# Kernel optimization log

Measured on AMD Instinct MI355X. Metric: run time of the kernel, lower is better.

Reference implementation:

```python
import jax, jax.numpy as jnp
import numpy as np

D_MODEL = 1024
N_HEADS = 16
D_K = D_MODEL // N_HEADS
D_FF = 4096
EPS = 1e-5


def setup_inputs() -> dict:
    key = jax.random.key(0)
    ks = jax.random.split(key, 16)
    s = 0.02
    d, f = D_MODEL, D_FF
    return {
        'ebd_x': jax.random.normal(ks[0], (2, 2048, d), jnp.float32),
        'Wq': jax.random.normal(ks[1], (d, d), jnp.float32) * s,
        'bq': jnp.zeros((d,), jnp.float32),
        'Wk': jax.random.normal(ks[2], (d, d), jnp.float32) * s,
        'bk': jnp.zeros((d,), jnp.float32),
        'Wv': jax.random.normal(ks[3], (d, d), jnp.float32) * s,
        'bv': jnp.zeros((d,), jnp.float32),
        'Wo': jax.random.normal(ks[4], (d, d), jnp.float32) * s,
        'bo': jnp.zeros((d,), jnp.float32),
        'W1': jax.random.normal(ks[5], (d, f), jnp.float32) * s,
        'b1': jnp.zeros((f,), jnp.float32),
        'W2': jax.random.normal(ks[6], (f, d), jnp.float32) * s,
        'b2': jnp.zeros((d,), jnp.float32),
        'g1': jnp.ones((d,), jnp.float32),
        'beta1': jnp.zeros((d,), jnp.float32),
        'g2': jnp.ones((d,), jnp.float32),
        'beta2': jnp.zeros((d,), jnp.float32),
    }


def _layernorm(x, g, b):
    mu = jnp.mean(x, axis=-1, keepdims=True)
    var = jnp.mean(jnp.square(x - mu), axis=-1, keepdims=True)
    return (x - mu) * jax.lax.rsqrt(var + EPS) * g + b


def reference(ebd_x, Wq, bq, Wk, bk, Wv, bv, Wo, bo, W1, b1, W2, b2, g1, beta1, g2, beta2):
    b, L, d = ebd_x.shape
    h, dk = N_HEADS, D_K
    # QKV projections, split heads: (b, h, L, dk)
    q = (ebd_x @ Wq + bq).reshape(b, L, h, dk).transpose(0, 2, 1, 3)
    k = (ebd_x @ Wk + bk).reshape(b, L, h, dk).transpose(0, 2, 1, 3)
    v = (ebd_x @ Wv + bv).reshape(b, L, h, dk).transpose(0, 2, 1, 3)
    scores = jnp.einsum('bhLd,bhld->bhLl', q, k) / jnp.sqrt(jnp.float32(dk))
    attn = jax.nn.softmax(scores, axis=-1)
    attn_v = jnp.einsum('bhLl,bhld->bhLd', attn, v)
    # faithful to source: reshape (b,h,L,dk) -> (b,L,d) WITHOUT transposing back
    attn_v = attn_v.reshape(b, L, d)
    attn_v = attn_v @ Wo + bo
    # dropout is identity in eval mode
    x1 = _layernorm(attn_v + ebd_x, g1, beta1)
    ff = jax.nn.gelu(x1 @ W1 + b1, approximate=False) @ W2 + b2
    return _layernorm(ff + x1, g2, beta2)
```

## Files before the change

### kernel.cpp

```cpp
#include <hip/hip_runtime.h>
#include <hip/hip_bf16.h>
#include <math.h>

typedef __bf16 bhalf;
typedef __bf16 bhalf8 __attribute__((ext_vector_type(8)));
typedef float  floatx4 __attribute__((ext_vector_type(4)));
typedef float  floatx8 __attribute__((ext_vector_type(8)));
typedef unsigned short ushort_t;
typedef unsigned short ushort8 __attribute__((ext_vector_type(8)));

#define MFMA16(a, b, c) __builtin_amdgcn_mfma_f32_16x16x32_bf16((a), (b), (c), 0, 0, 0)

__device__ __forceinline__ void gload_lds16(const bhalf* g, bhalf* l)
{
    __builtin_amdgcn_global_load_lds((const __attribute__((address_space(1))) void*)g,
                                     (__attribute__((address_space(3))) void*)l, 16, 0, 0);
}

enum { EPI_PLAIN = 0, EPI_RES = 1, EPI_GELU = 2, EPI_QKV = 3 };

__global__ __launch_bounds__(256) void detect_dtype(const ushort_t* __restrict__ x,
                                                    int* __restrict__ flag)
{
    __shared__ int tot;
    if (threadIdx.x == 0) tot = 0;
    __syncthreads();
    int cnt = 0;
#pragma unroll
    for (int it = 0; it < 8; ++it) {
        const ushort8 u = *(const ushort8*)(x + ((size_t)(it * 256 + threadIdx.x)) * 8);
#pragma unroll
        for (int j = 0; j < 8; j += 2) {
            const int e = (u[j] >> 7) & 0xFF;
            if (e >= 0x90) ++cnt;
        }
    }
    atomicAdd(&tot, cnt);
    __syncthreads();
    if (threadIdx.x == 0) flag[0] = (tot > 64) ? 1 : 0;
}

__global__ __launch_bounds__(256) void norm_x(const void* __restrict__ s,
                                              bhalf* __restrict__ d,
                                              const int* __restrict__ flag)
{
    const int i = (blockIdx.x * 256 + threadIdx.x) * 8;
    if (*flag) {
        const floatx8 v = *(const floatx8*)((const float*)s + i);
        bhalf8 o;
#pragma unroll
        for (int j = 0; j < 8; ++j) o[j] = (bhalf)v[j];
        *(bhalf8*)(d + i) = o;
    } else {
        *(ushort8*)((ushort_t*)d + i) = *(const ushort8*)((const ushort_t*)s + i);
    }
}

struct Cvt { const void* s; bhalf* d; int n; };
struct CvtArr { Cvt t[10]; };

__global__ __launch_bounds__(256) void norm_vec(CvtArr a, const int* __restrict__ flag)
{
    const Cvt c = a.t[blockIdx.y];
    const int i = (blockIdx.x * 256 + threadIdx.x) * 8;
    if (i >= c.n) return;
    if (*flag) {
        const floatx8 v = *(const floatx8*)((const float*)c.s + i);
        bhalf8 o;
#pragma unroll
        for (int j = 0; j < 8; ++j) o[j] = (bhalf)v[j];
        *(bhalf8*)(c.d + i) = o;
    } else {
        *(ushort8*)((ushort_t*)c.d + i) = *(const ushort8*)((const ushort_t*)c.s + i);
    }
}

struct TDesc { const void* src; bhalf* dst; int R, C; };
struct TDescArr { TDesc t[6]; };

__global__ __launch_bounds__(256) void transpose_all(TDescArr a, const int* __restrict__ flag)
{
    __shared__ bhalf sm[32][33];
    const int id = blockIdx.x;
    TDesc d;
    int rem;
    if (id < 4096)      { d = a.t[id >> 10]; rem = id & 1023; }
    else if (id < 8192) { d = a.t[4];        rem = id - 4096; }
    else                { d = a.t[5];        rem = id - 8192; }
    const int txc = d.C >> 5;
    const int bx = (rem % txc) * 32;
    const int by = (rem / txc) * 32;
    const int tx = threadIdx.x & 31;
    const int ty = threadIdx.x >> 5;
    if (*flag) {
        const float* fin = (const float*)d.src;
#pragma unroll
        for (int i = 0; i < 4; ++i)
            sm[ty + i * 8][tx] = (bhalf)fin[(size_t)(by + ty + i * 8) * d.C + bx + tx];
    } else {
        const bhalf* bin = (const bhalf*)d.src;
#pragma unroll
        for (int i = 0; i < 4; ++i)
            sm[ty + i * 8][tx] = bin[(size_t)(by + ty + i * 8) * d.C + bx + tx];
    }
    __syncthreads();
#pragma unroll
    for (int i = 0; i < 4; ++i)
        d.dst[(size_t)(bx + ty + i * 8) * d.R + by + tx] = sm[tx][ty + i * 8];
}

__global__ __launch_bounds__(256) void vt_transpose(const bhalf* __restrict__ Vw,
                                                    bhalf* __restrict__ Vt)
{
    __shared__ bhalf sm[32][33];
    const int bh = blockIdx.z;
    const int b = bh >> 4, h = bh & 15;
    const int tb = blockIdx.y * 32;
    const int db = blockIdx.x * 32;
    const int tx = threadIdx.x & 31;
    const int ty = threadIdx.x >> 5;
#pragma unroll
    for (int i = 0; i < 4; ++i)
        sm[ty + i * 8][tx] = Vw[(size_t)(b * 2048 + tb + ty + i * 8) * 1024 + h * 64 + db + tx];
    __syncthreads();
#pragma unroll
    for (int i = 0; i < 4; ++i)
        Vt[(size_t)(bh * 64 + db + ty + i * 8) * 2048 + tb + tx] = sm[tx][ty + i * 8];
}

template <int EPI, int TN>
__global__ __launch_bounds__(256) void gemm128(
    const bhalf* __restrict__ A, int lda,
    const bhalf* __restrict__ BT, int ldb,
    const bhalf* __restrict__ bias,
    const bhalf* __restrict__ resid,
    bhalf* __restrict__ C, int ldc, int K,
    bhalf* __restrict__ Ck, bhalf* __restrict__ Cv)
{
    __shared__ __align__(16) bhalf As[128 * 64];
    __shared__ __align__(16) bhalf Bs[TN * 64];

    const int tid  = threadIdx.x;
    const int lane = tid & 63;
    const int w    = tid >> 6;
    const int l15  = lane & 15;
    const int q    = lane >> 4;
    constexpr int MT = (TN == 128) ? 4 : 2;
    const int wm   = (TN == 128) ? (w >> 1) * 64 : w * 32;
    const int wn   = (TN == 128) ? (w & 1) * 64 : 0;
    const int n0   = blockIdx.x * TN;
    const int m0   = blockIdx.y * 128;

    const int r8 = lane >> 3;
    const int c8 = lane & 7;
    const int gc = (c8 ^ r8) << 3;

    floatx4 acc[MT][4];
#pragma unroll
    for (int i = 0; i < MT; ++i)
#pragma unroll
        for (int j = 0; j < 4; ++j) acc[i][j] = (floatx4){0.f, 0.f, 0.f, 0.f};

    for (int k0 = 0; k0 < K; k0 += 64) {
        __syncthreads();
#pragma unroll
        for (int i = 0; i < 4; ++i) {
            const int rb = w * 32 + i * 8;
            gload_lds16(A + (size_t)(m0 + rb + r8) * lda + k0 + gc, &As[rb * 64] + lane * 8);
        }
        if constexpr (TN == 128) {
#pragma unroll
            for (int i = 0; i < 4; ++i) {
                const int rb = w * 32 + i * 8;
                gload_lds16(BT + (size_t)(n0 + rb + r8) * ldb + k0 + gc, &Bs[rb * 64] + lane * 8);
            }
        } else {
#pragma unroll
            for (int i = 0; i < 2; ++i) {
                const int rb = w * 16 + i * 8;
                gload_lds16(BT + (size_t)(n0 + rb + r8) * ldb + k0 + gc, &Bs[rb * 64] + lane * 8);
            }
        }
        __syncthreads();
#pragma unroll
        for (int s = 0; s < 2; ++s) {
            const int pc = (((s * 4 + q) ^ (l15 & 7)) << 3);
            bhalf8 af[MT], bf[4];
#pragma unroll
            for (int mt = 0; mt < MT; ++mt)
                af[mt] = *(const bhalf8*)&As[(wm + mt * 16 + l15) * 64 + pc];
#pragma unroll
            for (int nt = 0; nt < 4; ++nt)
                bf[nt] = *(const bhalf8*)&Bs[(wn + nt * 16 + l15) * 64 + pc];
#pragma unroll
            for (int mt = 0; mt < MT; ++mt)
#pragma unroll
                for (int nt = 0; nt < 4; ++nt)
                    acc[mt][nt] = MFMA16(af[mt], bf[nt], acc[mt][nt]);
        }
    }

#pragma unroll
    for (int mt = 0; mt < MT; ++mt)
#pragma unroll
        for (int nt = 0; nt < 4; ++nt) {
            const int col = n0 + wn + nt * 16 + l15;
            const float bv = (float)bias[col];
#pragma unroll
            for (int r = 0; r < 4; ++r) {
                const int row = m0 + wm + mt * 16 + q * 4 + r;
                float v = acc[mt][nt][r] + bv;
                if constexpr (EPI == EPI_PLAIN) {
                    C[(size_t)row * ldc + col] = (bhalf)v;
                } else if constexpr (EPI == EPI_RES) {
                    v += (float)resid[(size_t)row * ldc + col];
                    C[(size_t)row * ldc + col] = (bhalf)v;
                } else if constexpr (EPI == EPI_GELU) {
                    v = 0.5f * v * (1.f + erff(v * 0.70710678118654752f));
                    C[(size_t)row * ldc + col] = (bhalf)v;
                } else {
                    if (col < 1024)       C [(size_t)row * 1024 + col]        = (bhalf)v;
                    else if (col < 2048)  Ck[(size_t)row * 1024 + col - 1024] = (bhalf)v;
                    else                  Cv[(size_t)row * 1024 + col - 2048] = (bhalf)v;
                }
            }
        }
}

template <int EPI>
__global__ __launch_bounds__(512, 2) void gemm256(
    const bhalf* __restrict__ A, int lda,
    const bhalf* __restrict__ BT, int ldb,
    const bhalf* __restrict__ bias,
    bhalf* __restrict__ C, int ldc, int K, int nbx,
    bhalf* __restrict__ Ck, bhalf* __restrict__ Cv)
{
    extern __shared__ __align__(16) bhalf sm[];

    const int tid  = threadIdx.x;
    const int lane = tid & 63;
    const int w    = tid >> 6;
    const int l15  = lane & 15;
    const int q    = lane >> 4;
    const int wm   = (w >> 2) * 128;
    const int wn   = (w & 3) * 64;
    const int w8   = w * 8;

    const int nwg = gridDim.x;
    const int cpx = nwg >> 3;
    const int id  = (blockIdx.x & 7) * cpx + (blockIdx.x >> 3);
    const int bx  = id % nbx;
    const int by  = id / nbx;
    const int n0  = bx * 256;
    const int m0  = by * 256;

    const int r8 = lane >> 3;
    const int c8 = lane & 7;
    const int gc = (c8 ^ r8) << 3;

    floatx4 acc[8][4];
#pragma unroll
    for (int i = 0; i < 8; ++i)
#pragma unroll
        for (int j = 0; j < 4; ++j) acc[i][j] = (floatx4){0.f, 0.f, 0.f, 0.f};

    auto stage = [&](int buf, int k0) {
        bhalf* as = sm + buf * 16384;
        bhalf* bs = sm + 32768 + buf * 16384;
#pragma unroll
        for (int i = 0; i < 4; ++i) {
            const int rb = i * 64 + w8;
            gload_lds16(A  + (size_t)(m0 + rb + r8) * lda + k0 + gc, as + rb * 64 + lane * 8);
            gload_lds16(BT + (size_t)(n0 + rb + r8) * ldb + k0 + gc, bs + rb * 64 + lane * 8);
        }
    };

    stage(0, 0);
    const int NT = K >> 6;
    for (int t = 0; t < NT; ++t) {
        const int cur = t & 1;
        const bhalf* as = sm + cur * 16384;
        const bhalf* bs = sm + 32768 + cur * 16384;
        __syncthreads();
        if (t + 1 < NT) stage(cur ^ 1, (t + 1) << 6);

#pragma unroll
        for (int ks = 0; ks < 2; ++ks) {
            const int pc = ((ks * 4 + q) ^ (l15 & 7)) << 3;
            bhalf8 bf[4];
#pragma unroll
            for (int nt = 0; nt < 4; ++nt)
                bf[nt] = *(const bhalf8*)&bs[(wn + nt * 16 + l15) * 64 + pc];
#pragma unroll
            for (int mh = 0; mh < 2; ++mh) {
                bhalf8 af[4];
#pragma unroll
                for (int mt = 0; mt < 4; ++mt)
                    af[mt] = *(const bhalf8*)&as[(wm + mh * 64 + mt * 16 + l15) * 64 + pc];
#pragma unroll
                for (int mt = 0; mt < 4; ++mt)
#pragma unroll
                    for (int nt = 0; nt < 4; ++nt)
                        acc[mh * 4 + mt][nt] = MFMA16(af[mt], bf[nt], acc[mh * 4 + mt][nt]);
            }
        }
    }

#pragma unroll
    for (int j = 0; j < 8; ++j)
#pragma unroll
        for (int nt = 0; nt < 4; ++nt) {
            const int col = n0 + wn + nt * 16 + l15;
            const float bv = (float)bias[col];
#pragma unroll
            for (int r = 0; r < 4; ++r) {
                const int row = m0 + wm + (j >> 2) * 64 + (j & 3) * 16 + q * 4 + r;
                float v = acc[j][nt][r] + bv;
                if constexpr (EPI == EPI_GELU) {
                    v = 0.5f * v * (1.f + erff(v * 0.70710678118654752f));
                    C[(size_t)row * ldc + col] = (bhalf)v;
                } else if constexpr (EPI == EPI_QKV) {
                    if (col < 1024)       C [(size_t)row * 1024 + col]        = (bhalf)v;
                    else if (col < 2048)  Ck[(size_t)row * 1024 + col - 1024] = (bhalf)v;
                    else                  Cv[(size_t)row * 1024 + col - 2048] = (bhalf)v;
                } else {
                    C[(size_t)row * ldc + col] = (bhalf)v;
                }
            }
        }
}

__global__ __launch_bounds__(256) void flash_attn(
    const bhalf* __restrict__ Q, const bhalf* __restrict__ Km,
    const bhalf* __restrict__ Vt, bhalf* __restrict__ ctx)
{
    __shared__ __align__(16) bhalf Ks[2][64 * 64];
    __shared__ __align__(16) bhalf Vs[2][64 * 64];

    const int tid  = threadIdx.x;
    const int lane = tid & 63;
    const int wq   = tid >> 6;
    const int l15  = lane & 15;
    const int q    = lane >> 4;
    const int bh   = blockIdx.x & 31;
    const int l0   = (blockIdx.x >> 5) * 64;
    const int b    = bh >> 4, h = bh & 15;
    const float SC = 0.125f * 1.44269504f;

    const bhalf* qp = Q + ((size_t)(b * 2048 + l0 + wq * 16 + l15)) * 1024 + h * 64 + q * 8;
    const bhalf8 aQ0 = *(const bhalf8*)qp;
    const bhalf8 aQ1 = *(const bhalf8*)(qp + 32);

    float ps = 0.f;
    floatx4 o[4];
#pragma unroll
    for (int ot = 0; ot < 4; ++ot) o[ot] = (floatx4){0.f, 0.f, 0.f, 0.f};

    const int r8 = lane >> 3;
    const int c8 = lane & 7;
    const bhalf* kbase = Km + ((size_t)(b * 2048)) * 1024 + h * 64;
    const bhalf* vbase = Vt + ((size_t)(bh * 64)) * 2048;

    auto stage = [&](int buf, int kt) {
#pragma unroll
        for (int i = 0; i < 2; ++i) {
            const int rb = wq * 16 + i * 8;
            const int fk = (((rb >> 3) << 1) ^ r8) & 7;
            gload_lds16(kbase + (size_t)(kt + rb + r8) * 1024 + ((c8 ^ fk) << 3),
                        &Ks[buf][rb * 64] + lane * 8);
            gload_lds16(vbase + (size_t)(rb + r8) * 2048 + kt + ((c8 ^ r8) << 3),
                        &Vs[buf][rb * 64] + lane * 8);
        }
    };

    stage(0, 0);
    int cur = 0;
    for (int kt = 0; kt < 2048; kt += 64) {
        __syncthreads();
        if (kt + 64 < 2048) stage(cur ^ 1, kt + 64);

        floatx4 s[4];
#pragma unroll
        for (int nt = 0; nt < 4; ++nt) {
            const int row = (nt >> 1) * 32 + (nt & 1) * 4 + ((l15 >> 2) << 3) + (l15 & 3);
            const int f = (((row >> 3) << 1) ^ row) & 7;
            const bhalf8 k0 = *(const bhalf8*)&Ks[cur][row * 64 + ((q ^ f) << 3)];
            const bhalf8 k1 = *(const bhalf8*)&Ks[cur][row * 64 + (((4 + q) ^ f) << 3)];
            floatx4 z = (floatx4){0.f, 0.f, 0.f, 0.f};
            z = MFMA16(k0, aQ0, z);
            s[nt] = MFMA16(k1, aQ1, z);
        }

        bhalf8 pa[2];
#pragma unroll
        for (int nt = 0; nt < 4; ++nt)
#pragma unroll
            for (int r = 0; r < 4; ++r) {
                const float pv = __builtin_amdgcn_exp2f(fmaf(s[nt][r], SC, -8.f));
                ps += pv;
                pa[nt >> 1][(nt & 1) * 4 + r] = (bhalf)pv;
            }

#pragma unroll
        for (int kc = 0; kc < 2; ++kc)
#pragma unroll
            for (int ot = 0; ot < 4; ++ot) {
                const bhalf8 bV = *(const bhalf8*)&Vs[cur][(ot * 16 + l15) * 64 + (((kc * 4 + q) ^ (l15 & 7)) << 3)];
                o[ot] = MFMA16(pa[kc], bV, o[ot]);
            }
        cur ^= 1;
    }

    ps += __shfl_xor(ps, 16);
    ps += __shfl_xor(ps, 32);
    const float invq = 1.f / ps;
    float inv[4];
#pragma unroll
    for (int r = 0; r < 4; ++r)
        inv[r] = __shfl(invq, (lane & 48) | (q * 4 + r));

#pragma unroll
    for (int ot = 0; ot < 4; ++ot)
#pragma unroll
        for (int r = 0; r < 4; ++r) {
            const int l = l0 + wq * 16 + q * 4 + r;
            const int kk = ot * 16 + l15;
            const int R = h * 128 + (l >> 4);
            const int Cc = (l & 15) * 64 + kk;
            ctx[((size_t)(b * 2048 + R)) * 1024 + Cc] = (bhalf)(o[ot][r] * inv[r]);
        }
}

__global__ __launch_bounds__(256) void ln_kernel(
    const bhalf* __restrict__ X, const bhalf* __restrict__ g,
    const bhalf* __restrict__ be, void* __restrict__ out, const int* __restrict__ flag)
{
    __shared__ float red[4][2];
    const int tid = threadIdx.x;
    const int wid = tid >> 6;
    const int rid = tid >> 7;
    const int lt  = tid & 127;
    const int row = blockIdx.x * 2 + rid;
    const int col = lt * 8;
    const bhalf8 xv = *(const bhalf8*)(X + (size_t)row * 1024 + col);
    float v[8], s1 = 0.f, s2 = 0.f;
#pragma unroll
    for (int i = 0; i < 8; ++i) {
        v[i] = (float)xv[i];
        s1 += v[i];
        s2 += v[i] * v[i];
    }
#pragma unroll
    for (int off = 1; off < 64; off <<= 1) {
        s1 += __shfl_xor(s1, off);
        s2 += __shfl_xor(s2, off);
    }
    if ((tid & 63) == 0) { red[wid][0] = s1; red[wid][1] = s2; }
    __syncthreads();
    const float t1 = red[rid * 2][0] + red[rid * 2 + 1][0];
    const float t2 = red[rid * 2][1] + red[rid * 2 + 1][1];
    const float mu = t1 * (1.f / 1024.f);
    const float rs = rsqrtf(t2 * (1.f / 1024.f) - mu * mu + 1e-5f);
    const bool f32 = flag && (*flag != 0);
    if (f32) {
        floatx8 ov;
#pragma unroll
        for (int i = 0; i < 8; ++i)
            ov[i] = ((v[i] - mu) * rs) * (float)g[col + i] + (float)be[col + i];
        *(floatx8*)((float*)out + (size_t)row * 1024 + col) = ov;
    } else {
        bhalf8 ov;
#pragma unroll
        for (int i = 0; i < 8; ++i)
            ov[i] = (bhalf)(((v[i] - mu) * rs) * (float)g[col + i] + (float)be[col + i]);
        *(bhalf8*)((bhalf*)out + (size_t)row * 1024 + col) = ov;
    }
}

extern "C" void kernel_launch(void* const* d_in, const int* in_sizes, int n_in,
                              void* d_out, int out_size, void* d_ws, size_t ws_size,
                              hipStream_t stream)
{
    (void)in_sizes; (void)n_in; (void)out_size; (void)ws_size;

    char* p = (char*)d_ws;
    const size_t MB = 1024 * 1024;
    int*   flag  = (int*)p;
    bhalf* vecs  = (bhalf*)(p + 128 * 1024);
    bhalf* Qw    = (bhalf*)(p + 1 * MB);
    bhalf* Kw    = (bhalf*)(p + 9 * MB);
    bhalf* Vw    = (bhalf*)(p + 17 * MB);
    bhalf* Vt    = (bhalf*)(p + 25 * MB);
    bhalf* x_n   = (bhalf*)(p + 33 * MB);
    bhalf* WqkvT = (bhalf*)(p + 41 * MB);
    bhalf* WoT   = (bhalf*)(p + 47 * MB);
    bhalf* W1T   = (bhalf*)(p + 49 * MB);
    bhalf* W2T   = (bhalf*)(p + 57 * MB);
    bhalf* ctx   = Vw;
    bhalf* ff1   = (bhalf*)(p + 17 * MB);
    bhalf* ln1   = Qw;
    bhalf* x1    = Kw;
    bhalf* ff2   = Qw;

    bhalf* bqkv  = vecs;
    bhalf* bo_n  = vecs + 1 * 4096;
    bhalf* b1_n  = vecs + 2 * 4096;
    bhalf* b2_n  = vecs + 3 * 4096;
    bhalf* g1_n  = vecs + 4 * 4096;
    bhalf* be1_n = vecs + 5 * 4096;
    bhalf* g2_n  = vecs + 6 * 4096;
    bhalf* be2_n = vecs + 7 * 4096;

    static bool attr_done = false;
    if (!attr_done) {
        hipFuncSetAttribute((const void*)gemm256<EPI_QKV>,
                            hipFuncAttributeMaxDynamicSharedMemorySize, 131072);
        hipFuncSetAttribute((const void*)gemm256<EPI_GELU>,
                            hipFuncAttributeMaxDynamicSharedMemorySize, 131072);
        attr_done = true;
    }

    const dim3 blk(256);
    const dim3 blk512(512);

    detect_dtype<<<1, blk, 0, stream>>>((const ushort_t*)d_in[0], flag);

    norm_x<<<2048, blk, 0, stream>>>(d_in[0], x_n, flag);
    CvtArr arr;
    arr.t[0] = {d_in[2],  bqkv,        1024};
    arr.t[1] = {d_in[4],  bqkv + 1024, 1024};
    arr.t[2] = {d_in[6],  bqkv + 2048, 1024};
    arr.t[3] = {d_in[8],  bo_n,        1024};
    arr.t[4] = {d_in[10], b1_n,        4096};
    arr.t[5] = {d_in[12], b2_n,        1024};
    arr.t[6] = {d_in[13], g1_n,        1024};
    arr.t[7] = {d_in[14], be1_n,       1024};
    arr.t[8] = {d_in[15], g2_n,        1024};
    arr.t[9] = {d_in[16], be2_n,       1024};
    norm_vec<<<dim3(2, 10), blk, 0, stream>>>(arr, flag);

    TDescArr td;
    td.t[0] = {d_in[1],  WqkvT,               1024, 1024};
    td.t[1] = {d_in[3],  WqkvT + 1024 * 1024, 1024, 1024};
    td.t[2] = {d_in[5],  WqkvT + 2048 * 1024, 1024, 1024};
    td.t[3] = {d_in[7],  WoT,                 1024, 1024};
    td.t[4] = {d_in[9],  W1T,                 1024, 4096};
    td.t[5] = {d_in[11], W2T,                 4096, 1024};
    transpose_all<<<12288, blk, 0, stream>>>(td, flag);

    gemm256<EPI_QKV><<<192, blk512, 131072, stream>>>(
        x_n, 1024, WqkvT, 1024, bqkv, Qw, 1024, 1024, 12, Kw, Vw);

    vt_transpose<<<dim3(2, 64, 32), blk, 0, stream>>>(Vw, Vt);

    flash_attn<<<1024, blk, 0, stream>>>(Qw, Kw, Vt, ctx);

    gemm128<EPI_RES, 64><<<dim3(16, 32), blk, 0, stream>>>(
        ctx, 1024, WoT, 1024, bo_n, x_n, ln1, 1024, 1024, nullptr, nullptr);
    ln_kernel<<<2048, blk, 0, stream>>>(ln1, g1_n, be1_n, x1, nullptr);

    gemm256<EPI_GELU><<<256, blk512, 131072, stream>>>(
        x1, 1024, W1T, 1024, b1_n, ff1, 4096, 1024, 16, nullptr, nullptr);
    gemm128<EPI_RES, 64><<<dim3(16, 32), blk, 0, stream>>>(
        ff1, 4096, W2T, 4096, b2_n, x1, ff2, 1024, 4096, nullptr, nullptr);
    ln_kernel<<<2048, blk, 0, stream>>>(ff2, g2_n, be2_n, d_out, flag);
}
```

Baseline: 369.9 us.

## Double-buffer LDS in gemm128 and remap blocks across XCDs

The 128x64 GEMM used for the output projection and the second FFN matmul now keeps two LDS buffers, so the async global-to-LDS load of the next K tile is issued before the current tile's MFMAs run. The single barrier per K step replaces the previous pair. A 1D grid with an XCD-aware block index remap groups neighbouring tiles on the same chiplet to improve L2 reuse. LDS use doubles to 48KB per block, which may cut occupancy, and the unused TN=128 and QKV-split variants are removed.

Result: slower. 441.6 us (+19.4%).

```diff
diff --git a/kernel.cpp b/kernel.cpp
--- a/kernel.cpp
+++ b/kernel.cpp
@@ -128,72 +128,72 @@
         Vt[(size_t)(bh * 64 + db + ty + i * 8) * 2048 + tb + tx] = sm[tx][ty + i * 8];
 }
 
-template <int EPI, int TN>
+template <int EPI>
 __global__ __launch_bounds__(256) void gemm128(
     const bhalf* __restrict__ A, int lda,
     const bhalf* __restrict__ BT, int ldb,
     const bhalf* __restrict__ bias,
     const bhalf* __restrict__ resid,
-    bhalf* __restrict__ C, int ldc, int K,
-    bhalf* __restrict__ Ck, bhalf* __restrict__ Cv)
-{
-    __shared__ __align__(16) bhalf As[128 * 64];
-    __shared__ __align__(16) bhalf Bs[TN * 64];
+    bhalf* __restrict__ C, int ldc, int K, int nbx)
+{
+    __shared__ __align__(16) bhalf As[2][128 * 64];
+    __shared__ __align__(16) bhalf Bs[2][64 * 64];
 
     const int tid  = threadIdx.x;
     const int lane = tid & 63;
     const int w    = tid >> 6;
     const int l15  = lane & 15;
     const int q    = lane >> 4;
-    constexpr int MT = (TN == 128) ? 4 : 2;
-    const int wm   = (TN == 128) ? (w >> 1) * 64 : w * 32;
-    const int wn   = (TN == 128) ? (w & 1) * 64 : 0;
-    const int n0   = blockIdx.x * TN;
-    const int m0   = blockIdx.y * 128;
+    const int wm   = w * 32;
+
+    const int nwg = gridDim.x;
+    const int cpx = nwg >> 3;
+    const int id  = (blockIdx.x & 7) * cpx + (blockIdx.x >> 3);
+    const int n0  = (id % nbx) * 64;
+    const int m0  = (id / nbx) * 128;
 
     const int r8 = lane >> 3;
     const int c8 = lane & 7;
     const int gc = (c8 ^ r8) << 3;
 
-    floatx4 acc[MT][4];
-#pragma unroll
-    for (int i = 0; i < MT; ++i)
+    floatx4 acc[2][4];
+#pragma unroll
+    for (int i = 0; i < 2; ++i)
 #pragma unroll
         for (int j = 0; j < 4; ++j) acc[i][j] = (floatx4){0.f, 0.f, 0.f, 0.f};
 
-    for (int k0 = 0; k0 < K; k0 += 64) {
-        __syncthreads();
+    auto stage = [&](int buf, int k0) {
 #pragma unroll
         for (int i = 0; i < 4; ++i) {
             const int rb = w * 32 + i * 8;
-            gload_lds16(A + (size_t)(m0 + rb + r8) * lda + k0 + gc, &As[rb * 64] + lane * 8);
-        }
-        if constexpr (TN == 128) {
-#pragma unroll
-            for (int i = 0; i < 4; ++i) {
-                const int rb = w * 32 + i * 8;
-                gload_lds16(BT + (size_t)(n0 + rb + r8) * ldb + k0 + gc, &Bs[rb * 64] + lane * 8);
-            }
-        } else {
-#pragma unroll
-            for (int i = 0; i < 2; ++i) {
-                const int rb = w * 16 + i * 8;
-                gload_lds16(BT + (size_t)(n0 + rb + r8) * ldb + k0 + gc, &Bs[rb * 64] + lane * 8);
-            }
-        }
+            gload_lds16(A + (size_t)(m0 + rb + r8) * lda + k0 + gc, &As[buf][rb * 64] + lane * 8);
+        }
+#pragma unroll
+        for (int i = 0; i < 2; ++i) {
+            const int rb = w * 16 + i * 8;
+            gload_lds16(BT + (size_t)(n0 + rb + r8) * ldb + k0 + gc, &Bs[buf][rb * 64] + lane * 8);
+        }
+    };
+
+    stage(0, 0);
+    const int NT = K >> 6;
+    for (int t = 0; t < NT; ++t) {
+        const int cur = t & 1;
         __syncthreads();
+        if (t + 1 < NT) stage(cur ^ 1, (t + 1) << 6);
+
 #pragma unroll
         for (int s = 0; s < 2; ++s) {
             const int pc = (((s * 4 + q) ^ (l15 & 7)) << 3);
-            bhalf8 af[MT], bf[4];
-#pragma unroll
-            for (int mt = 0; mt < MT; ++mt)
-                af[mt] = *(const bhalf8*)&As[(wm + mt * 16 + l15) * 64 + pc];
+            bhalf8 af[2], bf[4];
+#pragma unroll
+            for (int mt = 0; mt < 2; ++mt)
+                af[mt] = *(const bhalf8*)&As[cur][(wm + mt * 16 + l15) * 64 + pc];
 #pragma unroll
             for (int nt = 0; nt < 4; ++nt)
-                bf[nt] = *(const bhalf8*)&Bs[(wn + nt * 16 + l15) * 64 + pc];
-#pragma unroll
-            for (int mt = 0; mt < MT; ++mt)
+                bf[nt] = *(const bhalf8*)&Bs[cur][(nt * 16 + l15) * 64 + pc];
+#pragma unroll
+            for (int mt = 0; mt < 2; ++mt)
 #pragma unroll
                 for (int nt = 0; nt < 4; ++nt)
                     acc[mt][nt] = MFMA16(af[mt], bf[nt], acc[mt][nt]);
@@ -201,27 +201,23 @@
     }
 
 #pragma unroll
-    for (int mt = 0; mt < MT; ++mt)
+    for (int mt = 0; mt < 2; ++mt)
 #pragma unroll
         for (int nt = 0; nt < 4; ++nt) {
-            const int col = n0 + wn + nt * 16 + l15;
+            const int col = n0 + nt * 16 + l15;
             const float bv = (float)bias[col];
 #pragma unroll
             for (int r = 0; r < 4; ++r) {
                 const int row = m0 + wm + mt * 16 + q * 4 + r;
                 float v = acc[mt][nt][r] + bv;
-                if constexpr (EPI == EPI_PLAIN) {
-                    C[(size_t)row * ldc + col] = (bhalf)v;
-                } else if constexpr (EPI == EPI_RES) {
+                if constexpr (EPI == EPI_RES) {
                     v += (float)resid[(size_t)row * ldc + col];
                     C[(size_t)row * ldc + col] = (bhalf)v;
                 } else if constexpr (EPI == EPI_GELU) {
                     v = 0.5f * v * (1.f + erff(v * 0.70710678118654752f));
                     C[(size_t)row * ldc + col] = (bhalf)v;
                 } else {
-                    if (col < 1024)       C [(size_t)row * 1024 + col]        = (bhalf)v;
-                    else if (col < 2048)  Ck[(size_t)row * 1024 + col - 1024] = (bhalf)v;
-                    else                  Cv[(size_t)row * 1024 + col - 2048] = (bhalf)v;
+                    C[(size_t)row * ldc + col] = (bhalf)v;
                 }
             }
         }
@@ -555,13 +551,13 @@
 
     flash_attn<<<1024, blk, 0, stream>>>(Qw, Kw, Vt, ctx);
 
-    gemm128<EPI_RES, 64><<<dim3(16, 32), blk, 0, stream>>>(
-        ctx, 1024, WoT, 1024, bo_n, x_n, ln1, 1024, 1024, nullptr, nullptr);
+    gemm128<EPI_RES><<<512, blk, 0, stream>>>(
+        ctx, 1024, WoT, 1024, bo_n, x_n, ln1, 1024, 1024, 16);
     ln_kernel<<<2048, blk, 0, stream>>>(ln1, g1_n, be1_n, x1, nullptr);
 
     gemm256<EPI_GELU><<<256, blk512, 131072, stream>>>(
         x1, 1024, W1T, 1024, b1_n, ff1, 4096, 1024, 16, nullptr, nullptr);
-    gemm128<EPI_RES, 64><<<dim3(16, 32), blk, 0, stream>>>(
-        ff1, 4096, W2T, 4096, b2_n, x1, ff2, 1024, 4096, nullptr, nullptr);
+    gemm128<EPI_RES><<<512, blk, 0, stream>>>(
+        ff1, 4096, W2T, 4096, b2_n, x1, ff2, 1024, 4096, 16);
     ln_kernel<<<2048, blk, 0, stream>>>(ff2, g2_n, be2_n, d_out, flag);
 }
```
